# Optimization experiments

Hardware: AMD Instinct MI355X
Metric: run time of the kernel (lower is better)

## Reference

```python
import jax, jax.numpy as jnp
import numpy as np

IN_DIM = 512
OUT_DIM = 512
GRID_SIZE = 7
K = 4
N_KNOTS = GRID_SIZE + 2 * K + 1  # 16
N_BASIS = GRID_SIZE + K          # 11
BATCH = 16384


def b_splines(x, grid, k):
    # x: (B, in_dim), grid: (in_dim, N_KNOTS)
    x = x[..., None]  # (B, in, 1)
    value = ((x >= grid[:, :-1]) & (x < grid[:, 1:])).astype(x.dtype)  # (B, in, N_KNOTS-1)
    for p in range(1, k + 1):
        diff_left = grid[:, p:-1] - grid[:, :-(p + 1)]
        diff_right = grid[:, p + 1:] - grid[:, 1:-p]
        safe_dl = jnp.where(diff_left != 0, diff_left, 1.0)
        safe_dr = jnp.where(diff_right != 0, diff_right, 1.0)
        ratio_left = jnp.where(diff_left != 0, (x - grid[:, :-(p + 1)]) / safe_dl, 0.0)
        ratio_right = jnp.where(diff_right != 0, (grid[:, p + 1:] - x) / safe_dr, 0.0)
        value = (ratio_left * value[..., :-1] + ratio_right * value[..., 1:]) / (
            ratio_left + ratio_right + 1e-8)
    return value  # (B, in, N_BASIS)


def setup_inputs() -> dict:
    key = jax.random.key(0)
    k1, k2, k3, k4 = jax.random.split(key, 4)
    x = jax.random.uniform(k1, (BATCH, IN_DIM), dtype=jnp.float32)
    grid = jnp.tile(jnp.linspace(-1.0, 1.0, N_KNOTS, dtype=jnp.float32)[None, :], (IN_DIM, 1))
    coeff = jax.random.normal(k2, (OUT_DIM, IN_DIM, N_BASIS), dtype=jnp.float32) * 0.05
    scale_base = 1.0 / IN_DIM ** 0.5 + (
        jax.random.normal(k3, (OUT_DIM, IN_DIM), dtype=jnp.float32) * 2.0 - 1.0) * 0.05
    scale_spline = jnp.ones((OUT_DIM, IN_DIM), dtype=jnp.float32)
    bias = jnp.zeros((1, OUT_DIM), dtype=jnp.float32)
    return {"x": x, "grid": grid, "coeff": coeff, "scale_base": scale_base,
            "scale_spline": scale_spline, "bias": bias}


def reference(x, grid, coeff, scale_base, scale_spline, bias):
    shape = x.shape[:-1]
    x2 = x.reshape(-1, IN_DIM)
    splines = b_splines(x2, grid, K)                         # (B, in, N_BASIS)
    base_act = x2 + jnp.sin(x2)                              # KolmogorovActivation
    y_b = jnp.einsum('bi,oi->bo', base_act, scale_base)
    y_spline = jnp.einsum('bik,oik->bo', splines, coeff * scale_spline[:, :, None])
    y = y_b + y_spline + bias
    return y.reshape(*shape, OUT_DIM)
```

## Files before the change

kernel.cpp:

```cpp
#include <hip/hip_runtime.h>
#include <hip/hip_bf16.h>
#include <stdint.h>

#define IN_DIM  512
#define OUT_DIM 512
#define BATCH   16384
#define KPF     12
#define BM      128
#define BN      256
#define BK      96
#define KCH     64
#define TSTR    104
#define TILE_E  (BN * TSTR)

typedef __bf16 bf16;
typedef __bf16 bf16x8 __attribute__((ext_vector_type(8)));
typedef float  f32x4  __attribute__((ext_vector_type(4)));

__device__ __forceinline__ void gl2lds16(const void* g, void* l) {
    __builtin_amdgcn_global_load_lds((__attribute__((address_space(1))) uint32_t*)g,
                                     (__attribute__((address_space(3))) uint32_t*)l,
                                     16, 0, 0);
}
__device__ __forceinline__ uint bfbits(float v) {
    union { bf16 h; ushort u; } c; c.h = (bf16)v; return (uint)c.u;
}
__device__ __forceinline__ uint pk2(float lo, float hi) {
    return bfbits(lo) | (bfbits(hi) << 16);
}

__global__ void pack_w(const float* __restrict__ coeff,
                       const float* __restrict__ sbase,
                       const float* __restrict__ sspl,
                       bf16* __restrict__ W2) {
    __shared__ float cs[11 * 256];
    const int tid  = threadIdx.x;
    const int base = blockIdx.x * 256;
    const float* src = coeff + (size_t)base * 11;
#pragma unroll
    for (int j = 0; j < 11; ++j) cs[j * 256 + tid] = src[j * 256 + tid];
    __syncthreads();
    const int gid = base + tid;
    const int o = gid >> 9, i = gid & 511;
    const float s = sspl[gid];
    const float* cp = cs + tid * 11;
    union { bf16 hh[12]; uint2 uu[3]; } pk;
#pragma unroll
    for (int k = 0; k < 11; ++k) pk.hh[k] = (bf16)(cp[k] * s);
    pk.hh[11] = (bf16)sbase[gid];
    const int g = o >> 8, r = o & 255, kc = i >> 3, ic = i & 7;
    uint2* dst = (uint2*)(W2 + ((size_t)(g * 64 + kc) * 256 + r) * TSTR + ic * 12);
    dst[0] = pk.uu[0]; dst[1] = pk.uu[1]; dst[2] = pk.uu[2];
}

__global__ void __launch_bounds__(512, 2) kan_gemm(
    const float* __restrict__ xg,
    const float* __restrict__ gridp,
    const float* __restrict__ bias,
    const bf16*  __restrict__ W2,
    float* __restrict__ out)
{
    __shared__ bf16 Abuf[2 * BM * TSTR];
    __shared__ bf16 Bbuf[2 * BN * TSTR];

    const int tid  = threadIdx.x;
    const int lane = tid & 63;
    const int wave = tid >> 6;
    const int g  = blockIdx.x;
    const int n0 = g * BN;
    const int m0 = blockIdx.y * BM;

    const float g0    = gridp[0];
    const float inv_h = 1.0f / (gridp[1] - gridp[0]);

    const bf16* Wg = W2 + (size_t)g * KCH * TILE_E;
    const int nIss = (wave < 4) ? 7 : 6;

    const int row_e = tid & 127;
    const int fpair = tid >> 7;
    const float* xrow = xg + (size_t)(m0 + row_e) * IN_DIM + fpair * 2;

    const int wm = wave & 1, wn = wave >> 1;
    const int lr = lane & 15, lq = lane >> 4;

    f32x4 acc[4][4];
#pragma unroll
    for (int mt = 0; mt < 4; ++mt)
#pragma unroll
        for (int nt = 0; nt < 4; ++nt) { f32x4 z = {0.f, 0.f, 0.f, 0.f}; acc[mt][nt] = z; }

    auto evalOne = [&](float xv, uint* De) {
        float f  = __builtin_fmaf(xv, inv_h, -g0 * inv_h);
        f = fminf(fmaxf(f, 7.0f), 14.9999f);
        float fj = floorf(f);
        int   j0 = (int)fj;
        float t  = f - fj;
        float t1 = t + 1.0f, t2 = t + 2.0f, t3 = t + 3.0f;
        float s1 = 1.0f - t, s2 = 2.0f - t, s3 = 3.0f - t, s4 = 4.0f - t;
        float a0 = 0.5f * t, a1 = 0.5f * s1;
        const float i3 = (1.0f / 3.0f);
        float b0 = t  * a0 * i3;
        float b1 = (t1 * a1 + s2 * a0) * i3;
        float b2 = s1 * a1 * i3;
        float c0 = t  * b0 * 0.25f;
        float c1 = (t1 * b1 + s3 * b0) * 0.25f;
        float c2 = (t2 * b2 + s2 * b1) * 0.25f;
        float c3 = s1 * b2 * 0.25f;
        float w0 = t  * c0 * 0.2f;
        float w1 = (t1 * c1 + s4 * c0) * 0.2f;
        float w2 = (t2 * c2 + s3 * c1) * 0.2f;
        float w3 = (t3 * c3 + s2 * c2) * 0.2f;
        float w4 = s1 * c3 * 0.2f;
        const int q0 = j0 - 4;
        const int rr = q0 & 1;
        const int d  = q0 >> 1;
        uint P0 = pk2(w4, w3), P1 = pk2(w2, w1), P2 = bfbits(w0);
        uint A0 = rr ? (P0 << 16)                : P0;
        uint A1 = rr ? ((P0 >> 16) | (P1 << 16)) : P1;
        uint A2 = rr ? ((P1 >> 16) | (P2 << 16)) : P2;
        De[0] = 0u;
        De[1] = (d == 1) ? A0 : 0u;
        De[2] = (d == 2) ? A0 : ((d == 1) ? A1 : 0u);
        De[3] = (d == 3) ? A0 : ((d == 2) ? A1 : ((d == 1) ? A2 : 0u));
        De[4] = (d == 4) ? A0 : ((d == 3) ? A1 : ((d == 2) ? A2 : 0u));
        uint D5 = (d == 5) ? A0 : ((d == 4) ? A1 : ((d == 3) ? A2 : 0u));
        De[5] = (D5 & 0xFFFFu) | (bfbits(xv + __sinf(xv)) << 16);
    };
    auto evalPair = [&](float2 xc, bf16* Adst) {
        uint D[12];
        evalOne(xc.x, D);
        evalOne(xc.y, D + 6);
        uint4* awr = (uint4*)(Adst + row_e * TSTR + fpair * 24);
        awr[0] = make_uint4(D[0], D[1], D[2],  D[3]);
        awr[1] = make_uint4(D[4], D[5], D[6],  D[7]);
        awr[2] = make_uint4(D[8], D[9], D[10], D[11]);
    };
    auto dmaB = [&](int kc, bf16* Bdst) {
        const bf16* wsc = Wg + (size_t)kc * TILE_E;
#pragma unroll
        for (int j = 0; j < 7; ++j) {
            if (j < nIss) {
                int iss = wave + 8 * j;
                gl2lds16(wsc + iss * 512 + lane * 8, Bdst + iss * 512);
            }
        }
    };

    dmaB(0, Bbuf);
    float2 xb0 = *(const float2*)(xrow);
    float2 xb1 = *(const float2*)(xrow + 8);
    evalPair(xb0, Abuf);
    xb0 = *(const float2*)(xrow + 16);
    __syncthreads();

    for (int kc = 0; kc < KCH; ++kc) {
        const int p = kc & 1;
        if (kc < KCH - 1) {
            dmaB(kc + 1, Bbuf + (p ^ 1) * BN * TSTR);
            float2 xc = (kc & 1) ? xb0 : xb1;
            evalPair(xc, Abuf + (p ^ 1) * BM * TSTR);
            float2 xn = *(const float2*)(xrow + (((kc + 3) & (KCH - 1)) << 3));
            if (kc & 1) xb0 = xn; else xb1 = xn;
        }

        const bf16* Ap = Abuf + p * BM * TSTR;
        const bf16* Bp = Bbuf + p * BN * TSTR;
#pragma unroll
        for (int s = 0; s < 3; ++s) {
            bf16x8 af[4], bfr[4];
#pragma unroll
            for (int mt = 0; mt < 4; ++mt)
                af[mt] = *(const bf16x8*)&Ap[(wm * 64 + mt * 16 + lr) * TSTR + s * 32 + lq * 8];
#pragma unroll
            for (int nt = 0; nt < 4; ++nt)
                bfr[nt] = *(const bf16x8*)&Bp[(wn * 64 + nt * 16 + lr) * TSTR + s * 32 + lq * 8];
#pragma unroll
            for (int mt = 0; mt < 4; ++mt)
#pragma unroll
                for (int nt = 0; nt < 4; ++nt)
                    acc[mt][nt] = __builtin_amdgcn_mfma_f32_16x16x32_bf16(
                        af[mt], bfr[nt], acc[mt][nt], 0, 0, 0);
        }
        __syncthreads();
    }

#pragma unroll
    for (int nt = 0; nt < 4; ++nt) {
        const int gcol = n0 + wn * 64 + nt * 16 + lr;
        const float bv = bias[gcol];
#pragma unroll
        for (int mt = 0; mt < 4; ++mt) {
#pragma unroll
            for (int i = 0; i < 4; ++i) {
                const int grow = m0 + wm * 64 + mt * 16 + lq * 4 + i;
                out[(size_t)grow * OUT_DIM + gcol] = acc[mt][nt][i] + bv;
            }
        }
    }
}

extern "C" void kernel_launch(void* const* d_in, const int* in_sizes, int n_in,
                              void* d_out, int out_size, void* d_ws, size_t ws_size,
                              hipStream_t stream) {
    const float* x     = (const float*)d_in[0];
    const float* gridv = (const float*)d_in[1];
    const float* coeff = (const float*)d_in[2];
    const float* sbase = (const float*)d_in[3];
    const float* sspl  = (const float*)d_in[4];
    const float* bias  = (const float*)d_in[5];
    float* out = (float*)d_out;
    bf16*  W2  = (bf16*)d_ws;

    pack_w<<<dim3((OUT_DIM * IN_DIM) / 256), 256, 0, stream>>>(coeff, sbase, sspl, W2);
    kan_gemm<<<dim3(OUT_DIM / BN, BATCH / BM), 512, 0, stream>>>(x, gridv, bias, W2, out);
}
```

Measured before the change: 209.2 us.

## Split workgroup into producer and consumer waves for spline eval and MFMA

Waves 4-7 become producers: they issue the B-tile LDS DMA and evaluate the B-spline bases for the next K chunk. Waves 0-3 only do MFMA, each now covering a 64x128 output tile with 32 accumulators. The aim is to overlap VALU-heavy basis evaluation with matrix-core work instead of having every wave serialize both. In exchange only half the waves issue MFMAs, consumer register pressure doubles (128 accumulator floats), and occupancy may drop under the 512x2 launch bounds.

```diff
diff --git a/kernel.cpp b/kernel.cpp
--- a/kernel.cpp
+++ b/kernel.cpp
@@ -66,6 +66,7 @@
     const int tid  = threadIdx.x;
     const int lane = tid & 63;
     const int wave = tid >> 6;
+    const bool producer = (wave >= 4);
     const int g  = blockIdx.x;
     const int n0 = g * BN;
     const int m0 = blockIdx.y * BM;
@@ -74,20 +75,18 @@
     const float inv_h = 1.0f / (gridp[1] - gridp[0]);
 
     const bf16* Wg = W2 + (size_t)g * KCH * TILE_E;
-    const int nIss = (wave < 4) ? 7 : 6;
-
-    const int row_e = tid & 127;
-    const int fpair = tid >> 7;
-    const float* xrow = xg + (size_t)(m0 + row_e) * IN_DIM + fpair * 2;
-
-    const int wm = wave & 1, wn = wave >> 1;
+
+    const int pw    = wave & 3;
+    const int pt    = tid & 255;
+    const int row_e = pt & 127;
+    const int fq    = pt >> 7;
+    const float4* xp = (const float4*)(xg + (size_t)(m0 + row_e) * IN_DIM);
+
+    const int wm = wave & 1, wn = (wave >> 1) & 1;
     const int lr = lane & 15, lq = lane >> 4;
 
-    f32x4 acc[4][4];
-#pragma unroll
-    for (int mt = 0; mt < 4; ++mt)
-#pragma unroll
-        for (int nt = 0; nt < 4; ++nt) { f32x4 z = {0.f, 0.f, 0.f, 0.f}; acc[mt][nt] = z; }
+    f32x4 acc[4][8];
+    float4 xn;
 
     auto evalOne = [&](float xv, uint* De) {
         float f  = __builtin_fmaf(xv, inv_h, -g0 * inv_h);
@@ -126,74 +125,86 @@
         uint D5 = (d == 5) ? A0 : ((d == 4) ? A1 : ((d == 3) ? A2 : 0u));
         De[5] = (D5 & 0xFFFFu) | (bfbits(xv + __sinf(xv)) << 16);
     };
-    auto evalPair = [&](float2 xc, bf16* Adst) {
-        uint D[12];
-        evalOne(xc.x, D);
-        evalOne(xc.y, D + 6);
-        uint4* awr = (uint4*)(Adst + row_e * TSTR + fpair * 24);
-        awr[0] = make_uint4(D[0], D[1], D[2],  D[3]);
-        awr[1] = make_uint4(D[4], D[5], D[6],  D[7]);
-        awr[2] = make_uint4(D[8], D[9], D[10], D[11]);
+    auto evalQuad = [&](float4 xv, bf16* Adst) {
+        uint D[24];
+        evalOne(xv.x, D);
+        evalOne(xv.y, D + 6);
+        evalOne(xv.z, D + 12);
+        evalOne(xv.w, D + 18);
+        uint4* awr = (uint4*)(Adst + row_e * TSTR + fq * 48);
+        awr[0] = make_uint4(D[0],  D[1],  D[2],  D[3]);
+        awr[1] = make_uint4(D[4],  D[5],  D[6],  D[7]);
+        awr[2] = make_uint4(D[8],  D[9],  D[10], D[11]);
+        awr[3] = make_uint4(D[12], D[13], D[14], D[15]);
+        awr[4] = make_uint4(D[16], D[17], D[18], D[19]);
+        awr[5] = make_uint4(D[20], D[21], D[22], D[23]);
     };
     auto dmaB = [&](int kc, bf16* Bdst) {
         const bf16* wsc = Wg + (size_t)kc * TILE_E;
 #pragma unroll
-        for (int j = 0; j < 7; ++j) {
-            if (j < nIss) {
-                int iss = wave + 8 * j;
-                gl2lds16(wsc + iss * 512 + lane * 8, Bdst + iss * 512);
-            }
+        for (int j = 0; j < 13; ++j) {
+            const int iss = pw + 4 * j;
+            gl2lds16(wsc + iss * 512 + lane * 8, Bdst + iss * 512);
         }
     };
 
-    dmaB(0, Bbuf);
-    float2 xb0 = *(const float2*)(xrow);
-    float2 xb1 = *(const float2*)(xrow + 8);
-    evalPair(xb0, Abuf);
-    xb0 = *(const float2*)(xrow + 16);
+    if (producer) {
+        float4 xc = xp[fq];
+        xn = xp[2 + fq];
+        dmaB(0, Bbuf);
+        evalQuad(xc, Abuf);
+    } else {
+#pragma unroll
+        for (int mt = 0; mt < 4; ++mt)
+#pragma unroll
+            for (int nt = 0; nt < 8; ++nt) { f32x4 z = {0.f,0.f,0.f,0.f}; acc[mt][nt] = z; }
+    }
     __syncthreads();
 
     for (int kc = 0; kc < KCH; ++kc) {
         const int p = kc & 1;
-        if (kc < KCH - 1) {
-            dmaB(kc + 1, Bbuf + (p ^ 1) * BN * TSTR);
-            float2 xc = (kc & 1) ? xb0 : xb1;
-            evalPair(xc, Abuf + (p ^ 1) * BM * TSTR);
-            float2 xn = *(const float2*)(xrow + (((kc + 3) & (KCH - 1)) << 3));
-            if (kc & 1) xb0 = xn; else xb1 = xn;
-        }
-
-        const bf16* Ap = Abuf + p * BM * TSTR;
-        const bf16* Bp = Bbuf + p * BN * TSTR;
-#pragma unroll
-        for (int s = 0; s < 3; ++s) {
-            bf16x8 af[4], bfr[4];
-#pragma unroll
-            for (int mt = 0; mt < 4; ++mt)
-                af[mt] = *(const bf16x8*)&Ap[(wm * 64 + mt * 16 + lr) * TSTR + s * 32 + lq * 8];
-#pragma unroll
-            for (int nt = 0; nt < 4; ++nt)
-                bfr[nt] = *(const bf16x8*)&Bp[(wn * 64 + nt * 16 + lr) * TSTR + s * 32 + lq * 8];
-#pragma unroll
-            for (int mt = 0; mt < 4; ++mt)
-#pragma unroll
-                for (int nt = 0; nt < 4; ++nt)
-                    acc[mt][nt] = __builtin_amdgcn_mfma_f32_16x16x32_bf16(
-                        af[mt], bfr[nt], acc[mt][nt], 0, 0, 0);
+        if (producer) {
+            if (kc < KCH - 1) {
+                dmaB(kc + 1, Bbuf + (p ^ 1) * BN * TSTR);
+                float4 xt = xp[(((kc + 2) & (KCH - 1)) << 1) + fq];
+                evalQuad(xn, Abuf + (p ^ 1) * BM * TSTR);
+                xn = xt;
+            }
+        } else {
+            const bf16* Ap = Abuf + p * BM * TSTR;
+            const bf16* Bp = Bbuf + p * BN * TSTR;
+#pragma unroll
+            for (int s = 0; s < 3; ++s) {
+                bf16x8 af[4], bfv[8];
+#pragma unroll
+                for (int mt = 0; mt < 4; ++mt)
+                    af[mt] = *(const bf16x8*)&Ap[(wm * 64 + mt * 16 + lr) * TSTR + s * 32 + lq * 8];
+#pragma unroll
+                for (int nt = 0; nt < 8; ++nt)
+                    bfv[nt] = *(const bf16x8*)&Bp[(wn * 128 + nt * 16 + lr) * TSTR + s * 32 + lq * 8];
+#pragma unroll
+                for (int mt = 0; mt < 4; ++mt)
+#pragma unroll
+                    for (int nt = 0; nt < 8; ++nt)
+                        acc[mt][nt] = __builtin_amdgcn_mfma_f32_16x16x32_bf16(
+                            af[mt], bfv[nt], acc[mt][nt], 0, 0, 0);
+            }
         }
         __syncthreads();
     }
 
-#pragma unroll
-    for (int nt = 0; nt < 4; ++nt) {
-        const int gcol = n0 + wn * 64 + nt * 16 + lr;
-        const float bv = bias[gcol];
-#pragma unroll
-        for (int mt = 0; mt < 4; ++mt) {
-#pragma unroll
-            for (int i = 0; i < 4; ++i) {
-                const int grow = m0 + wm * 64 + mt * 16 + lq * 4 + i;
-                out[(size_t)grow * OUT_DIM + gcol] = acc[mt][nt][i] + bv;
+    if (!producer) {
+#pragma unroll
+        for (int nt = 0; nt < 8; ++nt) {
+            const int gcol = n0 + wn * 128 + nt * 16 + lr;
+            const float bv = bias[gcol];
+#pragma unroll
+            for (int mt = 0; mt < 4; ++mt) {
+#pragma unroll
+                for (int i = 0; i < 4; ++i) {
+                    const int grow = m0 + wm * 64 + mt * 16 + lq * 4 + i;
+                    out[(size_t)grow * OUT_DIM + gcol] = acc[mt][nt][i] + bv;
+                }
             }
         }
     }
```

New measurement: 190.3 us. 9.0% less time.

## Load B fragments directly from pre-swizzled global into registers, skip LDS

Applied to the files above, without the earlier changes.

The weight pack kernel now writes weights in MFMA fragment order, so each wave can load its B operands straight from global memory into registers instead of staging them through LDS with global_load_lds. The B shared buffer is removed, the loop is unrolled by two with register double buffering, and half the waves issue MFMA before spline evaluation while the other half evaluate first, with s_setprio around the MFMA bursts. This removes LDS traffic and LDS footprint for B, but raises VGPR pressure from 24 bf16x8 B registers and relies on L2 to serve the redundant weight reads.

```diff
diff --git a/kernel.cpp b/kernel.cpp
--- a/kernel.cpp
+++ b/kernel.cpp
@@ -5,23 +5,18 @@
 #define IN_DIM  512
 #define OUT_DIM 512
 #define BATCH   16384
-#define KPF     12
 #define BM      128
 #define BN      256
 #define BK      96
 #define KCH     64
 #define TSTR    104
-#define TILE_E  (BN * TSTR)
+#define TILE_U  3072
+#define TILE_EL 24576
 
 typedef __bf16 bf16;
 typedef __bf16 bf16x8 __attribute__((ext_vector_type(8)));
 typedef float  f32x4  __attribute__((ext_vector_type(4)));
 
-__device__ __forceinline__ void gl2lds16(const void* g, void* l) {
-    __builtin_amdgcn_global_load_lds((__attribute__((address_space(1))) uint32_t*)g,
-                                     (__attribute__((address_space(3))) uint32_t*)l,
-                                     16, 0, 0);
-}
 __device__ __forceinline__ uint bfbits(float v) {
     union { bf16 h; ushort u; } c; c.h = (bf16)v; return (uint)c.u;
 }
@@ -32,36 +27,83 @@
 __global__ void pack_w(const float* __restrict__ coeff,
                        const float* __restrict__ sbase,
                        const float* __restrict__ sspl,
-                       bf16* __restrict__ W2) {
-    __shared__ float cs[11 * 256];
-    const int tid  = threadIdx.x;
-    const int base = blockIdx.x * 256;
-    const float* src = coeff + (size_t)base * 11;
-#pragma unroll
-    for (int j = 0; j < 11; ++j) cs[j * 256 + tid] = src[j * 256 + tid];
+                       bf16* __restrict__ W3) {
+    __shared__ __align__(16) bf16 L[256 * 96];
+    const int t  = threadIdx.x;
+    const int g  = blockIdx.x >> 6;
+    const int kc = blockIdx.x & 63;
+    const int o  = g * 256 + t;
+    const float* cp = coeff + ((size_t)o * 512 + kc * 8) * 11;
+    const float* sp = sspl  + (size_t)o * 512 + kc * 8;
+    const float* bp = sbase + (size_t)o * 512 + kc * 8;
+    union { bf16 h[96]; uint4 q[12]; } rw;
+#pragma unroll
+    for (int il = 0; il < 8; ++il) {
+        const float s = sp[il];
+#pragma unroll
+        for (int k = 0; k < 11; ++k) rw.h[il * 12 + k] = (bf16)(cp[il * 11 + k] * s);
+        rw.h[il * 12 + 11] = (bf16)bp[il];
+    }
+    uint4* lrow = (uint4*)(L + t * 96);
+#pragma unroll
+    for (int j = 0; j < 12; ++j) lrow[j] = rw.q[j];
     __syncthreads();
-    const int gid = base + tid;
-    const int o = gid >> 9, i = gid & 511;
-    const float s = sspl[gid];
-    const float* cp = cs + tid * 11;
-    union { bf16 hh[12]; uint2 uu[3]; } pk;
-#pragma unroll
-    for (int k = 0; k < 11; ++k) pk.hh[k] = (bf16)(cp[k] * s);
-    pk.hh[11] = (bf16)sbase[gid];
-    const int g = o >> 8, r = o & 255, kc = i >> 3, ic = i & 7;
-    uint2* dst = (uint2*)(W2 + ((size_t)(g * 64 + kc) * 256 + r) * TSTR + ic * 12);
-    dst[0] = pk.uu[0]; dst[1] = pk.uu[1]; dst[2] = pk.uu[2];
-}
+    uint4* dst = (uint4*)W3 + (size_t)(g * 64 + kc) * TILE_U;
+#pragma unroll
+    for (int uu = 0; uu < 12; ++uu) {
+        const int U   = uu * 256 + t;
+        const int rb  = U / 192;
+        const int rem = U - rb * 192;
+        const int s   = rem >> 6;
+        const int li  = rem & 63;
+        const int lq  = li >> 4, lr = li & 15;
+        dst[U] = *(const uint4*)(L + (rb * 16 + lr) * 96 + s * 32 + lq * 8);
+    }
+}
+
+
+#define LOAD_B(Barr, kcn)                                                     \
+  {                                                                           \
+    const bf16* _bb = WgB + (size_t)(kcn) * TILE_EL + boff;                   \
+    _Pragma("unroll")                                                         \
+    for (int f = 0; f < 12; ++f)                                              \
+      Barr[f] = *(const bf16x8*)(_bb + (f / 3) * 1536 + (f % 3) * 512);       \
+  }
+
+#define EVALP(kcn, Adst)                                                      \
+  {                                                                           \
+    float2 _xc = xn;                                                          \
+    xn = *(const float2*)(xrow + ((((kcn) + 1) & 63) << 3));                  \
+    evalPair(_xc, (Adst));                                                    \
+  }
+
+#define MFMA_PH(Ap, Barr)                                                     \
+  {                                                                           \
+    _Pragma("unroll")                                                         \
+    for (int s = 0; s < 3; ++s) {                                             \
+      bf16x8 af[4];                                                           \
+      _Pragma("unroll")                                                       \
+      for (int mt = 0; mt < 4; ++mt)                                          \
+        af[mt] = *(const bf16x8*)&(Ap)[(wm * 64 + mt * 16 + lr) * TSTR + s * 32 + lq * 8]; \
+      __builtin_amdgcn_s_setprio(1);                                          \
+      _Pragma("unroll")                                                       \
+      for (int mt = 0; mt < 4; ++mt)                                          \
+        _Pragma("unroll")                                                     \
+        for (int nt = 0; nt < 4; ++nt)                                        \
+          acc[mt][nt] = __builtin_amdgcn_mfma_f32_16x16x32_bf16(              \
+              af[mt], Barr[nt * 3 + s], acc[mt][nt], 0, 0, 0);                \
+      __builtin_amdgcn_s_setprio(0);                                          \
+    }                                                                         \
+  }
 
 __global__ void __launch_bounds__(512, 2) kan_gemm(
     const float* __restrict__ xg,
     const float* __restrict__ gridp,
     const float* __restrict__ bias,
-    const bf16*  __restrict__ W2,
+    const bf16*  __restrict__ W3,
     float* __restrict__ out)
 {
     __shared__ bf16 Abuf[2 * BM * TSTR];
-    __shared__ bf16 Bbuf[2 * BN * TSTR];
 
     const int tid  = threadIdx.x;
     const int lane = tid & 63;
@@ -73,8 +115,7 @@
     const float g0    = gridp[0];
     const float inv_h = 1.0f / (gridp[1] - gridp[0]);
 
-    const bf16* Wg = W2 + (size_t)g * KCH * TILE_E;
-    const int nIss = (wave < 4) ? 7 : 6;
+    const bf16* WgB = W3 + (size_t)g * KCH * TILE_EL;
 
     const int row_e = tid & 127;
     const int fpair = tid >> 7;
@@ -82,12 +123,20 @@
 
     const int wm = wave & 1, wn = wave >> 1;
     const int lr = lane & 15, lq = lane >> 4;
+    const bool mfirst = (wave >= 4);
+    const int boff = wn * 6144 + lane * 8;
+
+    bf16* const Ab0 = Abuf;
+    bf16* const Ab1 = Abuf + BM * TSTR;
 
     f32x4 acc[4][4];
 #pragma unroll
     for (int mt = 0; mt < 4; ++mt)
 #pragma unroll
         for (int nt = 0; nt < 4; ++nt) { f32x4 z = {0.f, 0.f, 0.f, 0.f}; acc[mt][nt] = z; }
+
+    bf16x8 Bc[12], Bn[12];
+    float2 xn;
 
     auto evalOne = [&](float xv, uint* De) {
         float f  = __builtin_fmaf(xv, inv_h, -g0 * inv_h);
@@ -135,53 +184,29 @@
         awr[1] = make_uint4(D[4], D[5], D[6],  D[7]);
         awr[2] = make_uint4(D[8], D[9], D[10], D[11]);
     };
-    auto dmaB = [&](int kc, bf16* Bdst) {
-        const bf16* wsc = Wg + (size_t)kc * TILE_E;
-#pragma unroll
-        for (int j = 0; j < 7; ++j) {
-            if (j < nIss) {
-                int iss = wave + 8 * j;
-                gl2lds16(wsc + iss * 512 + lane * 8, Bdst + iss * 512);
-            }
+
+    LOAD_B(Bc, 0);
+    {
+        float2 xc0 = *(const float2*)(xrow);
+        xn = *(const float2*)(xrow + 8);
+        evalPair(xc0, Ab0);
+    }
+    __syncthreads();
+
+    for (int it = 0; it < 32; ++it) {
+        const int kc0 = 2 * it;
+        LOAD_B(Bn, kc0 + 1);
+        if (mfirst) { MFMA_PH(Ab0, Bc); EVALP(kc0 + 1, Ab1); }
+        else        { EVALP(kc0 + 1, Ab1); MFMA_PH(Ab0, Bc); }
+        __syncthreads();
+        if (it < 31) {
+            LOAD_B(Bc, kc0 + 2);
+            if (mfirst) { MFMA_PH(Ab1, Bn); EVALP(kc0 + 2, Ab0); }
+            else        { EVALP(kc0 + 2, Ab0); MFMA_PH(Ab1, Bn); }
+            __syncthreads();
+        } else {
+            MFMA_PH(Ab1, Bn);
         }
-    };
-
-    dmaB(0, Bbuf);
-    float2 xb0 = *(const float2*)(xrow);
-    float2 xb1 = *(const float2*)(xrow + 8);
-    evalPair(xb0, Abuf);
-    xb0 = *(const float2*)(xrow + 16);
-    __syncthreads();
-
-    for (int kc = 0; kc < KCH; ++kc) {
-        const int p = kc & 1;
-        if (kc < KCH - 1) {
-            dmaB(kc + 1, Bbuf + (p ^ 1) * BN * TSTR);
-            float2 xc = (kc & 1) ? xb0 : xb1;
-            evalPair(xc, Abuf + (p ^ 1) * BM * TSTR);
-            float2 xn = *(const float2*)(xrow + (((kc + 3) & (KCH - 1)) << 3));
-            if (kc & 1) xb0 = xn; else xb1 = xn;
-        }
-
-        const bf16* Ap = Abuf + p * BM * TSTR;
-        const bf16* Bp = Bbuf + p * BN * TSTR;
-#pragma unroll
-        for (int s = 0; s < 3; ++s) {
-            bf16x8 af[4], bfr[4];
-#pragma unroll
-            for (int mt = 0; mt < 4; ++mt)
-                af[mt] = *(const bf16x8*)&Ap[(wm * 64 + mt * 16 + lr) * TSTR + s * 32 + lq * 8];
-#pragma unroll
-            for (int nt = 0; nt < 4; ++nt)
-                bfr[nt] = *(const bf16x8*)&Bp[(wn * 64 + nt * 16 + lr) * TSTR + s * 32 + lq * 8];
-#pragma unroll
-            for (int mt = 0; mt < 4; ++mt)
-#pragma unroll
-                for (int nt = 0; nt < 4; ++nt)
-                    acc[mt][nt] = __builtin_amdgcn_mfma_f32_16x16x32_bf16(
-                        af[mt], bfr[nt], acc[mt][nt], 0, 0, 0);
-        }
-        __syncthreads();
     }
 
 #pragma unroll
@@ -209,8 +234,8 @@
     const float* sspl  = (const float*)d_in[4];
     const float* bias  = (const float*)d_in[5];
     float* out = (float*)d_out;
-    bf16*  W2  = (bf16*)d_ws;
-
-    pack_w<<<dim3((OUT_DIM * IN_DIM) / 256), 256, 0, stream>>>(coeff, sbase, sspl, W2);
-    kan_gemm<<<dim3(OUT_DIM / BN, BATCH / BM), 512, 0, stream>>>(x, gridv, bias, W2, out);
-}
+    bf16*  W3  = (bf16*)d_ws;
+
+    pack_w<<<dim3(128), 256, 0, stream>>>(coeff, sbase, sspl, W3);
+    kan_gemm<<<dim3(OUT_DIM / BN, BATCH / BM), 512, 0, stream>>>(x, gridv, bias, W3, out);
+}
```

Result: slower. 573.5 us (+174.2%).
